# Performance work log

Hardware: AMD Instinct MI355X
Metric: run time of the kernel (lower is better)

Reference implementation:

```python
import jax, jax.numpy as jnp
import numpy as np

N_USERS = 1_000_000
AVG_DEG = 32
E = N_USERS * AVG_DEG
K = 5
IN_F = 1
OUT_F = 64
BN_EPS = 1e-5


def setup_inputs() -> dict:
    key = jax.random.key(0)
    ks = jax.random.split(key, 6)
    stdv = 1.0 / np.sqrt(IN_F * K)
    return {
        "x": jax.random.normal(ks[0], (N_USERS, IN_F), dtype=jnp.float32),
        "edge_index": jax.random.randint(ks[1], (2, E), 0, N_USERS, dtype=jnp.int32),
        "edge_weight": jax.random.uniform(ks[2], (E,), dtype=jnp.float32),
        "weight": jax.random.uniform(ks[3], (OUT_F, K, IN_F), dtype=jnp.float32, minval=-stdv, maxval=stdv),
        "bias": jax.random.uniform(ks[4], (OUT_F,), dtype=jnp.float32, minval=-stdv, maxval=stdv),
        "gamma": jnp.ones((N_USERS,), dtype=jnp.float32),
        "beta": jnp.zeros((N_USERS,), dtype=jnp.float32),
    }


def reference(x, edge_index, edge_weight, weight, bias, gamma, beta):
    N = x.shape[0]
    src, dst = edge_index[0], edge_index[1]
    # K-hop propagation: gather x_j, scale by edge_weight, scatter-add at dst
    feats = [x]
    cur = x
    for _ in range(K - 1):
        msg = cur[src] * edge_weight[:, None]                 # [E, IN_F]
        cur = jax.ops.segment_sum(msg, dst, num_segments=N)   # [N, IN_F]
        feats.append(cur)
    # [N, K*IN_F], hop-major / feature-minor ordering (matches torch reshape)
    conv = jnp.concatenate(feats, axis=1)[None]               # [1, N, K*IN_F]
    h = weight.reshape(OUT_F, K * IN_F).T                     # [K*IN_F, OUT_F]
    y = jnp.matmul(conv, h) + bias                            # [1, N, OUT_F]
    # BatchNorm1d(N_users) in training mode: stats over (batch, feature) per node-channel
    mean = jnp.mean(y, axis=(0, 2), keepdims=True)
    var = jnp.mean((y - mean) ** 2, axis=(0, 2), keepdims=True)  # biased var
    y_hat = (y - mean) * jax.lax.rsqrt(var + BN_EPS)
    return y_hat * gamma[None, :, None] + beta[None, :, None]
```

## Files before the change

kernel.cpp:

```cpp
#include <hip/hip_runtime.h>

#define N_USERS 1000000
#define NEDGE   32000000
#define OUT_F   64
#define BN_EPS  1e-5f

#define SBITS     12
#define S_BUCKET  4096
#define NB        245
#define CAP       136896
#define SCAT_BLOCKS 1024
#define TILE      4096
#define NTILES    ((NEDGE + TILE - 1) / TILE)

#define SUP_B     6
#define NSUP      41
#define S_SUPER   24576
#define NWIN      245
#define NBINS2    (NSUP * NWIN)
#define HSPLIT    6
#define RGRID     1024
#define MT        34

static_assert((unsigned long long)NEDGE * 8ull ==
              (unsigned long long)N_USERS * OUT_F * 4ull,
              "compact rec2 must exactly fit d_out");

typedef unsigned int uint4v __attribute__((ext_vector_type(4)));
typedef unsigned int uint2v __attribute__((ext_vector_type(2)));
typedef int          int4v  __attribute__((ext_vector_type(4)));
typedef float        flt4v  __attribute__((ext_vector_type(4)));


__global__ void init_cursors(unsigned* __restrict__ cursors) {
    int i = blockIdx.x * blockDim.x + threadIdx.x;
    if (i < NB) cursors[i] = (unsigned)i * CAP;
}

__global__ __launch_bounds__(256) void scatter_bin(
    const int* __restrict__ src, const int* __restrict__ dst,
    const float* __restrict__ ew, uint2* __restrict__ rec,
    unsigned* __restrict__ cursors) {
    __shared__ uint2 srec[TILE];
    __shared__ unsigned short sbkt[TILE];
    __shared__ unsigned hist[NB];
    __shared__ unsigned curs[NB];
    __shared__ unsigned gpos[NB];
    __shared__ unsigned chunkT[256];
    int tid = threadIdx.x;

    for (int tile = blockIdx.x; tile < NTILES; tile += gridDim.x) {
        int e0 = tile * TILE;
        int n_this = (e0 + TILE <= NEDGE) ? TILE : (NEDGE - e0);
        int nq = n_this >> 2;
        int q0 = e0 >> 2;

        for (int i = tid; i < NB; i += 256) hist[i] = 0;
        __syncthreads();

        int4v dv[4]; int4v sv[4]; flt4v wv[4];
        #pragma unroll
        for (int k = 0; k < 4; ++k) {
            int q = k * 256 + tid;
            if (q < nq) {
                dv[k] = __builtin_nontemporal_load(reinterpret_cast<const int4v*>(dst) + q0 + q);
                sv[k] = __builtin_nontemporal_load(reinterpret_cast<const int4v*>(src) + q0 + q);
                wv[k] = __builtin_nontemporal_load(reinterpret_cast<const flt4v*>(ew) + q0 + q);
            }
        }
        #pragma unroll
        for (int k = 0; k < 4; ++k) {
            int q = k * 256 + tid;
            if (q < nq) {
                #pragma unroll
                for (int j = 0; j < 4; ++j)
                    atomicAdd(&hist[dv[k][j] >> SBITS], 1u);
            }
        }
        __syncthreads();

        {
            int base = tid * 4;
            unsigned run = 0;
            #pragma unroll
            for (int k = 0; k < 4; ++k) {
                int idx = base + k;
                unsigned v = (idx < NB) ? hist[idx] : 0u;
                if (idx < NB) hist[idx] = run;
                run += v;
            }
            chunkT[tid] = run;
        }
        __syncthreads();
        if (tid == 0) {
            unsigned r = 0;
            for (int t = 0; t < 256; ++t) { unsigned v = chunkT[t]; chunkT[t] = r; r += v; }
        }
        __syncthreads();
        {
            int base = tid * 4;
            unsigned add = chunkT[tid];
            #pragma unroll
            for (int k = 0; k < 4; ++k) {
                int idx = base + k;
                if (idx < NB) hist[idx] += add;
            }
        }
        __syncthreads();

        for (int b = tid; b < NB; b += 256) {
            unsigned st = hist[b];
            unsigned en = (b == NB - 1) ? (unsigned)n_this : hist[b + 1];
            unsigned c = en - st;
            gpos[b] = c ? atomicAdd(&cursors[b], c) : 0u;
            curs[b] = 0;
        }
        __syncthreads();

        #pragma unroll
        for (int k = 0; k < 4; ++k) {
            int q = k * 256 + tid;
            if (q < nq) {
                #pragma unroll
                for (int j = 0; j < 4; ++j) {
                    int dd = dv[k][j], ss = sv[k][j];
                    int b = dd >> SBITS;
                    unsigned p = hist[b] + atomicAdd(&curs[b], 1u);
                    srec[p] = make_uint2(((unsigned)(dd & (S_BUCKET - 1)) << 20) | (unsigned)ss,
                                         __float_as_uint(wv[k][j]));
                    sbkt[p] = (unsigned short)b;
                }
            }
        }
        __syncthreads();

        for (int i = tid; i < n_this; i += 256) {
            unsigned b = sbkt[i];
            rec[gpos[b] + ((unsigned)i - hist[b])] = srec[i];
        }
        __syncthreads();
    }
}


__global__ __launch_bounds__(256) void count_bins(
    const uint2* __restrict__ rec, const unsigned* __restrict__ cursors,
    unsigned* __restrict__ cnt2) {
    __shared__ unsigned hist[NWIN];
    int tid = threadIdx.x;
    int b = blockIdx.x >> 2, q = blockIdx.x & 3;
    for (int i = tid; i < NWIN; i += 256) hist[i] = 0;
    __syncthreads();
    unsigned cnt = cursors[b] - (unsigned)b * CAP;
    unsigned lo = (unsigned)(((unsigned long long)cnt * (unsigned)q) >> 2) & ~1u;
    unsigned hi = (q == 3) ? (cnt & ~1u)
                           : ((unsigned)(((unsigned long long)cnt * (unsigned)(q + 1)) >> 2) & ~1u);
    const uint2* bp = rec + (size_t)b * CAP;

    unsigned i = lo + 2u * (unsigned)tid;
    for (; i + 1538u <= hi; i += 2048u) {
        uint4v v0 = __builtin_nontemporal_load(reinterpret_cast<const uint4v*>(bp + i));
        uint4v v1 = __builtin_nontemporal_load(reinterpret_cast<const uint4v*>(bp + i + 512));
        uint4v v2 = __builtin_nontemporal_load(reinterpret_cast<const uint4v*>(bp + i + 1024));
        uint4v v3 = __builtin_nontemporal_load(reinterpret_cast<const uint4v*>(bp + i + 1536));
        atomicAdd(&hist[(v0.x & 0xFFFFFu) >> 12], 1u);
        atomicAdd(&hist[(v0.z & 0xFFFFFu) >> 12], 1u);
        atomicAdd(&hist[(v1.x & 0xFFFFFu) >> 12], 1u);
        atomicAdd(&hist[(v1.z & 0xFFFFFu) >> 12], 1u);
        atomicAdd(&hist[(v2.x & 0xFFFFFu) >> 12], 1u);
        atomicAdd(&hist[(v2.z & 0xFFFFFu) >> 12], 1u);
        atomicAdd(&hist[(v3.x & 0xFFFFFu) >> 12], 1u);
        atomicAdd(&hist[(v3.z & 0xFFFFFu) >> 12], 1u);
    }
    for (; i + 2u <= hi; i += 512u) {
        uint4v v = __builtin_nontemporal_load(reinterpret_cast<const uint4v*>(bp + i));
        atomicAdd(&hist[(v.x & 0xFFFFFu) >> 12], 1u);
        atomicAdd(&hist[(v.z & 0xFFFFFu) >> 12], 1u);
    }
    if (q == 3 && (cnt & 1u) && tid == 0) {
        uint2v r = __builtin_nontemporal_load(
            reinterpret_cast<const uint2v*>(bp + (cnt - 1u)));
        atomicAdd(&hist[(r.x & 0xFFFFFu) >> 12], 1u);
    }
    __syncthreads();
    unsigned base = (unsigned)(b / SUP_B) * (unsigned)NWIN;
    for (int k = tid; k < NWIN; k += 256)
        if (hist[k]) atomicAdd(&cnt2[base + k], hist[k]);
}


__global__ __launch_bounds__(256) void prefix_bins(
    const unsigned* __restrict__ cnt2, unsigned* __restrict__ bases,
    unsigned* __restrict__ cursors2) {
    __shared__ unsigned chunkT[256];
    int t = threadIdx.x;
    unsigned loc[40];
    unsigned run = 0;
    for (int k = 0; k < 40; ++k) {
        int idx = t * 40 + k;
        unsigned v = (idx < NBINS2) ? cnt2[idx] : 0u;
        loc[k] = run; run += v;
    }
    chunkT[t] = run;
    __syncthreads();
    if (t == 0) {
        unsigned r = 0;
        for (int i = 0; i < 256; ++i) { unsigned v = chunkT[i]; chunkT[i] = r; r += v; }
    }
    __syncthreads();
    unsigned add = chunkT[t];
    for (int k = 0; k < 40; ++k) {
        int idx = t * 40 + k;
        if (idx < NBINS2) { unsigned v = loc[k] + add; bases[idx] = v; cursors2[idx] = v; }
    }
    if (t == 0) bases[NBINS2] = (unsigned)NEDGE;
}


__global__ __launch_bounds__(256) void regroup(
    const uint2* __restrict__ rec, const unsigned* __restrict__ cursors,
    uint2* __restrict__ rec2, unsigned* __restrict__ cursors2) {
    __shared__ uint2 srec[TILE];
    __shared__ unsigned char skey[TILE];
    __shared__ unsigned hist[NWIN];
    __shared__ unsigned curs[NWIN];
    __shared__ unsigned gpos[NWIN];
    __shared__ unsigned chunkT[256];
    int tid = threadIdx.x;

    for (int ti = blockIdx.x; ti < NB * MT; ti += gridDim.x) {
        int b = ti / MT;
        unsigned t = (unsigned)(ti % MT);
        unsigned cntb = cursors[b] - (unsigned)b * CAP;
        unsigned e0 = t * TILE;
        if (e0 >= cntb) continue;
        unsigned n_this = (cntb - e0 < TILE) ? (cntb - e0) : TILE;
        unsigned binbase = (unsigned)(b / SUP_B) * (unsigned)NWIN;
        unsigned rb = (unsigned)(b % SUP_B) << 12;
        const uint2* bp = rec + (size_t)b * CAP;

        for (int i = tid; i < NWIN; i += 256) hist[i] = 0;
        __syncthreads();

        uint4v rv[8];
        #pragma unroll
        for (int k2 = 0; k2 < 8; ++k2) {
            unsigned idx = (unsigned)(k2 * 512 + tid * 2);
            if (idx < n_this)
                rv[k2] = __builtin_nontemporal_load(
                    reinterpret_cast<const uint4v*>(bp + e0 + idx));
        }
        #pragma unroll
        for (int k2 = 0; k2 < 8; ++k2) {
            unsigned idx = (unsigned)(k2 * 512 + tid * 2);
            if (idx < n_this)     atomicAdd(&hist[(rv[k2].x & 0xFFFFFu) >> 12], 1u);
            if (idx + 1 < n_this) atomicAdd(&hist[(rv[k2].z & 0xFFFFFu) >> 12], 1u);
        }
        __syncthreads();

        chunkT[tid] = (tid < NWIN) ? hist[tid] : 0u;
        __syncthreads();
        if (tid == 0) {
            unsigned r = 0;
            for (int i = 0; i < 256; ++i) { unsigned v = chunkT[i]; chunkT[i] = r; r += v; }
        }
        __syncthreads();
        if (tid < NWIN) hist[tid] = chunkT[tid];
        __syncthreads();
        if (tid < NWIN) {
            unsigned st = hist[tid];
            unsigned en = (tid == NWIN - 1) ? n_this : hist[tid + 1];
            unsigned c = en - st;
            gpos[tid] = c ? atomicAdd(&cursors2[binbase + tid], c) : 0u;
            curs[tid] = 0;
        }
        __syncthreads();

        #pragma unroll
        for (int k2 = 0; k2 < 8; ++k2) {
            unsigned idx = (unsigned)(k2 * 512 + tid * 2);
            if (idx < n_this) {
                unsigned m = rv[k2].x;
                unsigned k = (m & 0xFFFFFu) >> 12;
                unsigned p = hist[k] + atomicAdd(&curs[k], 1u);
                srec[p] = make_uint2((((m >> 20) + rb) << 12) | (m & 0xFFFu), rv[k2].y);
                skey[p] = (unsigned char)k;
            }
            if (idx + 1 < n_this) {
                unsigned m = rv[k2].z;
                unsigned k = (m & 0xFFFFFu) >> 12;
                unsigned p = hist[k] + atomicAdd(&curs[k], 1u);
                srec[p] = make_uint2((((m >> 20) + rb) << 12) | (m & 0xFFFu), rv[k2].w);
                skey[p] = (unsigned char)k;
            }
        }
        __syncthreads();

        for (unsigned i = (unsigned)tid; i < n_this; i += 256) {
            unsigned k = skey[i];
            rec2[gpos[k] + (i - hist[k])] = srec[i];
        }
        __syncthreads();
    }
}


__global__ __launch_bounds__(512) void hop_super(
    const uint2* __restrict__ rec2, const unsigned* __restrict__ bases,
    const float* __restrict__ cur, float* __restrict__ nxt) {
    __shared__ float acc[S_SUPER];
    int tid = threadIdx.x;
    int s = blockIdx.x / HSPLIT;
    int j = blockIdx.x % HSPLIT;
    for (int i = tid; i < S_SUPER; i += 512) acc[i] = 0.0f;
    __syncthreads();

    const unsigned* bs = bases + s * NWIN;
    for (int k = j; k < NWIN; k += HSPLIT) {
        unsigned lo = bs[k];
        unsigned hi = bs[k + 1];
        const float* win = cur + ((size_t)k << 12);
        unsigned i = lo + (unsigned)tid;
        for (; i + 1536u < hi; i += 2048u) {
            uint2 r0 = rec2[i];
            uint2 r1 = rec2[i + 512u];
            uint2 r2 = rec2[i + 1024u];
            uint2 r3 = rec2[i + 1536u];
            float c0 = win[r0.x & 0xFFFu];
            float c1 = win[r1.x & 0xFFFu];
            float c2 = win[r2.x & 0xFFFu];
            float c3 = win[r3.x & 0xFFFu];
            atomicAdd(&acc[r0.x >> 12], c0 * __uint_as_float(r0.y));
            atomicAdd(&acc[r1.x >> 12], c1 * __uint_as_float(r1.y));
            atomicAdd(&acc[r2.x >> 12], c2 * __uint_as_float(r2.y));
            atomicAdd(&acc[r3.x >> 12], c3 * __uint_as_float(r3.y));
        }
        for (; i < hi; i += 512u) {
            uint2 r = rec2[i];
            atomicAdd(&acc[r.x >> 12], win[r.x & 0xFFFu] * __uint_as_float(r.y));
        }
        __syncthreads();
    }
    int d0 = s * S_SUPER;
    for (int i = tid; i < S_SUPER; i += 512) {
        int n = d0 + i;
        if (n < N_USERS) atomicAdd(&nxt[n], acc[i]);
    }
}


__global__ void zero_kernel(float* __restrict__ p, int n) {
    int i = blockIdx.x * blockDim.x + threadIdx.x;
    int stride = gridDim.x * blockDim.x;
    for (; i < n; i += stride) p[i] = 0.0f;
}

__global__ __launch_bounds__(256) void hop_atomic(
    const int* __restrict__ src, const int* __restrict__ dst,
    const float* __restrict__ ew, const float* __restrict__ cur,
    float* __restrict__ nxt) {
    int e = blockIdx.x * blockDim.x + threadIdx.x;
    if (e * 4 < NEDGE) {
        int4   s = ((const int4*)src)[e];
        int4   d = ((const int4*)dst)[e];
        float4 w = ((const float4*)ew)[e];
        atomicAdd(&nxt[d.x], cur[s.x] * w.x);
        atomicAdd(&nxt[d.y], cur[s.y] * w.y);
        atomicAdd(&nxt[d.z], cur[s.z] * w.z);
        atomicAdd(&nxt[d.w], cur[s.w] * w.w);
    }
}


__global__ __launch_bounds__(256) void finalize_kernel(
    const float* __restrict__ x,  const float* __restrict__ f1,
    const float* __restrict__ f2, const float* __restrict__ f3,
    const float* __restrict__ f4, const float* __restrict__ W,
    const float* __restrict__ bias, const float* __restrict__ gamma,
    const float* __restrict__ beta, float* __restrict__ out) {
    int lane = threadIdx.x & 63;
    int waveInBlock = threadIdx.x >> 6;
    int wavesPerBlock = blockDim.x >> 6;
    int gwave  = blockIdx.x * wavesPerBlock + waveInBlock;
    int nwaves = gridDim.x * wavesPerBlock;

    float w0 = W[lane * 5 + 0];
    float w1 = W[lane * 5 + 1];
    float w2 = W[lane * 5 + 2];
    float w3 = W[lane * 5 + 3];
    float w4 = W[lane * 5 + 4];
    float b  = bias[lane];

    for (int n = gwave; n < N_USERS; n += nwaves) {
        float c0 = x[n], c1 = f1[n], c2 = f2[n], c3 = f3[n], c4 = f4[n];
        float y = b + c0 * w0 + c1 * w1 + c2 * w2 + c3 * w3 + c4 * w4;

        float s = y;
        #pragma unroll
        for (int off = 32; off; off >>= 1) s += __shfl_xor(s, off);
        float mean = s * (1.0f / 64.0f);

        float d = y - mean;
        float v = d * d;
        #pragma unroll
        for (int off = 32; off; off >>= 1) v += __shfl_xor(v, off);
        float var = v * (1.0f / 64.0f);

        float o = d * rsqrtf(var + BN_EPS) * gamma[n] + beta[n];
        __builtin_nontemporal_store(o, &out[(size_t)n * OUT_F + lane]);
    }
}

extern "C" void kernel_launch(void* const* d_in, const int* in_sizes, int n_in,
                              void* d_out, int out_size, void* d_ws, size_t ws_size,
                              hipStream_t stream) {
    const float* x     = (const float*)d_in[0];
    const int*   ei    = (const int*)d_in[1];
    const float* ew    = (const float*)d_in[2];
    const float* W     = (const float*)d_in[3];
    const float* bias  = (const float*)d_in[4];
    const float* gamma = (const float*)d_in[5];
    const float* beta  = (const float*)d_in[6];
    float* out = (float*)d_out;

    const int* src = ei;
    const int* dst = ei + NEDGE;

    float* f = (float*)d_ws;
    uint2* rec = (uint2*)(f + 4ull * N_USERS);
    unsigned* cursors  = (unsigned*)(rec + (size_t)NB * CAP);
    unsigned* cnt2     = cursors + 1024;
    unsigned* bases    = cnt2 + 10240;
    unsigned* cursors2 = bases + 10240;
    size_t needed = 16000000ull + (size_t)NB * CAP * 8 + 4096 + 3ull * 40960;

    uint2* rec2 = (uint2*)d_out;

    if (ws_size >= needed) {
        init_cursors<<<1, 256, 0, stream>>>(cursors);
        zero_kernel<<<2048, 256, 0, stream>>>(f, 4 * N_USERS);
        zero_kernel<<<40, 256, 0, stream>>>((float*)cnt2, NBINS2);
        scatter_bin<<<SCAT_BLOCKS, 256, 0, stream>>>(src, dst, ew, rec, cursors);
        count_bins<<<NB * 4, 256, 0, stream>>>(rec, cursors, cnt2);
        prefix_bins<<<1, 256, 0, stream>>>(cnt2, bases, cursors2);
        regroup<<<RGRID, 256, 0, stream>>>(rec, cursors, rec2, cursors2);
        const float* cur = x;
        for (int h = 0; h < 4; ++h) {
            float* nxt = f + (size_t)h * N_USERS;
            hop_super<<<NSUP * HSPLIT, 512, 0, stream>>>(rec2, bases, cur, nxt);
            cur = nxt;
        }
    } else {
        zero_kernel<<<4096, 256, 0, stream>>>(f, 4 * N_USERS);
        const float* cur = x;
        for (int h = 0; h < 4; ++h) {
            float* nxt = f + (size_t)h * N_USERS;
            hop_atomic<<<NEDGE / 4 / 256, 256, 0, stream>>>(src, dst, ew, cur, nxt);
            cur = nxt;
        }
    }

    finalize_kernel<<<2048, 256, 0, stream>>>(
        x, f, f + N_USERS, f + 2 * N_USERS, f + 3 * N_USERS,
        W, bias, gamma, beta, out);
}
```

Before: 1.757 ms.

## Assign hop windows per wavefront, halve superblock size, deepen gather unroll

The hop kernel now gives each 64-lane wavefront its own source window instead of having the whole 512-thread block sweep one window with a block barrier after every window. Superblocks shrink to 12288 nodes (82 of them), which halves the LDS accumulator, and the split per superblock rises to 8 blocks. The inner loop unrolls 16 independent record loads and gathers to keep more memory traffic in flight. In exchange there are twice as many bins, a larger prefix scan and more global atomics at flush, and per-window load imbalance across wavefronts may now matter.

```diff
diff --git a/kernel.cpp b/kernel.cpp
--- a/kernel.cpp
+++ b/kernel.cpp
@@ -13,12 +13,12 @@
 #define TILE      4096
 #define NTILES    ((NEDGE + TILE - 1) / TILE)
 
-#define SUP_B     6
-#define NSUP      41
-#define S_SUPER   24576
+#define SUP_B     3
+#define NSUP      82
+#define S_SUPER   12288
 #define NWIN      245
 #define NBINS2    (NSUP * NWIN)
-#define HSPLIT    6
+#define HSPLIT    8
 #define RGRID     1024
 #define MT        34
 
@@ -194,10 +194,10 @@
     unsigned* __restrict__ cursors2) {
     __shared__ unsigned chunkT[256];
     int t = threadIdx.x;
-    unsigned loc[40];
+    unsigned loc[79];
     unsigned run = 0;
-    for (int k = 0; k < 40; ++k) {
-        int idx = t * 40 + k;
+    for (int k = 0; k < 79; ++k) {
+        int idx = t * 79 + k;
         unsigned v = (idx < NBINS2) ? cnt2[idx] : 0u;
         loc[k] = run; run += v;
     }
@@ -209,8 +209,8 @@
     }
     __syncthreads();
     unsigned add = chunkT[t];
-    for (int k = 0; k < 40; ++k) {
-        int idx = t * 40 + k;
+    for (int k = 0; k < 79; ++k) {
+        int idx = t * 79 + k;
         if (idx < NBINS2) { unsigned v = loc[k] + add; bases[idx] = v; cursors2[idx] = v; }
     }
     if (t == 0) bases[NBINS2] = (unsigned)NEDGE;
@@ -315,32 +315,42 @@
     for (int i = tid; i < S_SUPER; i += 512) acc[i] = 0.0f;
     __syncthreads();
 
+    int wid = tid >> 6;
+    int lane = tid & 63;
+    int slot = j * 8 + wid;
     const unsigned* bs = bases + s * NWIN;
-    for (int k = j; k < NWIN; k += HSPLIT) {
+
+    for (int k = slot; k < NWIN; k += HSPLIT * 8) {
         unsigned lo = bs[k];
         unsigned hi = bs[k + 1];
         const float* win = cur + ((size_t)k << 12);
-        unsigned i = lo + (unsigned)tid;
-        for (; i + 1536u < hi; i += 2048u) {
-            uint2 r0 = rec2[i];
-            uint2 r1 = rec2[i + 512u];
-            uint2 r2 = rec2[i + 1024u];
-            uint2 r3 = rec2[i + 1536u];
-            float c0 = win[r0.x & 0xFFFu];
-            float c1 = win[r1.x & 0xFFFu];
-            float c2 = win[r2.x & 0xFFFu];
-            float c3 = win[r3.x & 0xFFFu];
-            atomicAdd(&acc[r0.x >> 12], c0 * __uint_as_float(r0.y));
-            atomicAdd(&acc[r1.x >> 12], c1 * __uint_as_float(r1.y));
-            atomicAdd(&acc[r2.x >> 12], c2 * __uint_as_float(r2.y));
-            atomicAdd(&acc[r3.x >> 12], c3 * __uint_as_float(r3.y));
-        }
-        for (; i < hi; i += 512u) {
+        unsigned i = lo + (unsigned)lane;
+        for (; i + 15u * 64u < hi; i += 16u * 64u) {
+            uint2 r[16];
+            #pragma unroll
+            for (int q = 0; q < 16; ++q) r[q] = rec2[i + (unsigned)q * 64u];
+            float c[16];
+            #pragma unroll
+            for (int q = 0; q < 16; ++q) c[q] = win[r[q].x & 0xFFFu];
+            #pragma unroll
+            for (int q = 0; q < 16; ++q)
+                atomicAdd(&acc[r[q].x >> 12], c[q] * __uint_as_float(r[q].y));
+        }
+        for (; i + 3u * 64u < hi; i += 4u * 64u) {
+            uint2 r[4];
+            #pragma unroll
+            for (int q = 0; q < 4; ++q) r[q] = rec2[i + (unsigned)q * 64u];
+            #pragma unroll
+            for (int q = 0; q < 4; ++q)
+                atomicAdd(&acc[r[q].x >> 12],
+                          win[r[q].x & 0xFFFu] * __uint_as_float(r[q].y));
+        }
+        for (; i < hi; i += 64u) {
             uint2 r = rec2[i];
             atomicAdd(&acc[r.x >> 12], win[r.x & 0xFFFu] * __uint_as_float(r.y));
         }
-        __syncthreads();
-    }
+    }
+    __syncthreads();
     int d0 = s * S_SUPER;
     for (int i = tid; i < S_SUPER; i += 512) {
         int n = d0 + i;
@@ -430,16 +440,16 @@
     uint2* rec = (uint2*)(f + 4ull * N_USERS);
     unsigned* cursors  = (unsigned*)(rec + (size_t)NB * CAP);
     unsigned* cnt2     = cursors + 1024;
-    unsigned* bases    = cnt2 + 10240;
-    unsigned* cursors2 = bases + 10240;
-    size_t needed = 16000000ull + (size_t)NB * CAP * 8 + 4096 + 3ull * 40960;
+    unsigned* bases    = cnt2 + 20480;
+    unsigned* cursors2 = bases + 20480;
+    size_t needed = 16000000ull + (size_t)NB * CAP * 8 + 4096 + 3ull * 81920;
 
     uint2* rec2 = (uint2*)d_out;
 
     if (ws_size >= needed) {
         init_cursors<<<1, 256, 0, stream>>>(cursors);
         zero_kernel<<<2048, 256, 0, stream>>>(f, 4 * N_USERS);
-        zero_kernel<<<40, 256, 0, stream>>>((float*)cnt2, NBINS2);
+        zero_kernel<<<80, 256, 0, stream>>>((float*)cnt2, NBINS2);
         scatter_bin<<<SCAT_BLOCKS, 256, 0, stream>>>(src, dst, ew, rec, cursors);
         count_bins<<<NB * 4, 256, 0, stream>>>(rec, cursors, cnt2);
         prefix_bins<<<1, 256, 0, stream>>>(cnt2, bases, cursors2);
```

New measurement: 1.764 ms. About the same (+0.4%).
